# Kernel optimization log

Measured on AMD Instinct MI355X. Metric: run time of the kernel, lower is better.

## Reference

```python
import jax, jax.numpy as jnp
import numpy as np

NEG_SLOPE = 0.2  # GAT LeakyReLU slope
NEG_INF = -1e9


def setup_inputs() -> dict:
    key = jax.random.key(0)
    ks = jax.random.split(key, 5)
    B, N, D = 16, 1024, 256
    H, F = 4, 64  # heads, per-head out dim (out_dim=256)
    x = jax.random.normal(ks[0], (B, N, D), dtype=jnp.float32)
    adj = jax.random.uniform(ks[1], (B, N, N), dtype=jnp.float32)
    W = jax.random.normal(ks[2], (D, H * F), dtype=jnp.float32) * (1.0 / np.sqrt(D))
    a_src = jax.random.normal(ks[3], (H, F), dtype=jnp.float32) * (1.0 / np.sqrt(F))
    a_dst = jax.random.normal(ks[4], (H, F), dtype=jnp.float32) * (1.0 / np.sqrt(F))
    bias = jnp.zeros((H * F,), dtype=jnp.float32)
    return {"x": x, "adj": adj, "W": W, "a_src": a_src, "a_dst": a_dst, "bias": bias}


def reference(x, adj, W, a_src, a_dst, bias):
    B, N, D = x.shape
    H, F = a_src.shape
    # Linear transform per head: [B,N,H,F]
    h = jnp.einsum("bnd,dhf->bnhf", x, W.reshape(D, H, F))
    # Attention logit components: [B,N,H]
    e_src = jnp.einsum("bnhf,hf->bnh", h, a_src)
    e_dst = jnp.einsum("bnhf,hf->bnh", h, a_dst)
    # logits[b,i,j,h]: target i gathers from source j (edge = adj[b,i,j] > 0.5)
    logits = e_dst[:, :, None, :] + e_src[:, None, :, :]
    logits = jnp.where(logits >= 0, logits, NEG_SLOPE * logits)  # LeakyReLU
    mask = adj > 0.5  # [B,N,N]
    logits = jnp.where(mask[..., None], logits, NEG_INF)
    att = jax.nn.softmax(logits, axis=2)  # softmax over source neighbors j
    out = jnp.einsum("bijh,bjhf->bihf", att, h)  # aggregate
    return out.reshape(B, N, H * F) + bias  # concat heads
```

## Files before the change

### kernel.cpp

```cpp
#include <hip/hip_runtime.h>

typedef __bf16 bf16x8 __attribute__((ext_vector_type(8)));
typedef float f32x4 __attribute__((ext_vector_type(4)));

constexpr int Bsz = 16;
constexpr int Nsz = 1024;
constexpr int Dsz = 256;
constexpr int Hsz = 4;
constexpr int HFsz = 256;
constexpr int BN = Bsz * Nsz;

__device__ __forceinline__ unsigned f2bf(float f) {
    unsigned u = __float_as_uint(f);
    return (u + 0x7FFFu + ((u >> 16) & 1u)) >> 16;
}

__global__ __launch_bounds__(256) void wcvt(const float* __restrict__ Wm,
                                            unsigned short* __restrict__ WbT) {
    const int t = threadIdx.x;
    const int c = blockIdx.x * 4 + (t >> 6);
    const int d0 = (t & 63) * 4;
    const float v0 = Wm[(size_t)(d0 + 0) * HFsz + c];
    const float v1 = Wm[(size_t)(d0 + 1) * HFsz + c];
    const float v2 = Wm[(size_t)(d0 + 2) * HFsz + c];
    const float v3 = Wm[(size_t)(d0 + 3) * HFsz + c];
    uint2 pk;
    pk.x = f2bf(v0) | (f2bf(v1) << 16);
    pk.y = f2bf(v2) | (f2bf(v3) << 16);
    *(uint2*)&WbT[(size_t)c * Dsz + d0] = pk;
}

__global__ __launch_bounds__(256) void gat_h_e3(
    const float* __restrict__ x,
    const unsigned short* __restrict__ WbT,
    const float* __restrict__ a_src,
    const float* __restrict__ a_dst,
    unsigned short* __restrict__ hT,
    float* __restrict__ esrcT,
    float* __restrict__ edstT)
{
    const int n0g = blockIdx.x * 32, b = n0g >> 10, n0 = n0g & 1023;
    const int t = threadIdx.x, lane = t & 63, w = t >> 6;
    const int m = lane & 15, q = lane >> 4;

    __shared__ alignas(16) unsigned short Lds[4 * 64 * 40];

    const float4* x4 = (const float4*)(x + (size_t)n0g * Dsz);
#pragma unroll
    for (int i = 0; i < 8; ++i) {
        const int f = t + 256 * i;
        const int row = f >> 6, d4 = (f & 63) * 4;
        const float4 xv = x4[f];
        uint2 pk;
        pk.x = f2bf(xv.x) | (f2bf(xv.y) << 16);
        pk.y = f2bf(xv.z) | (f2bf(xv.w) << 16);
        *(uint2*)&Lds[row * 264 + d4] = pk;
    }
    __syncthreads();

    const unsigned short* Ab = WbT + (size_t)(w * 64 + m) * Dsz + q * 8;
    f32x4 acc[4][2];
#pragma unroll
    for (int ht = 0; ht < 4; ++ht)
#pragma unroll
        for (int nt = 0; nt < 2; ++nt) acc[ht][nt] = (f32x4){0.f, 0.f, 0.f, 0.f};

#pragma unroll
    for (int kk = 0; kk < 8; ++kk) {
        const int k0 = kk * 32;
        const bf16x8 bfr0 = *(const bf16x8*)&Lds[(0 * 16 + m) * 264 + k0 + q * 8];
        const bf16x8 bfr1 = *(const bf16x8*)&Lds[(1 * 16 + m) * 264 + k0 + q * 8];
#pragma unroll
        for (int ht = 0; ht < 4; ++ht) {
            const bf16x8 afr = *(const bf16x8*)&Ab[ht * 16 * Dsz + k0];
            acc[ht][0] = __builtin_amdgcn_mfma_f32_16x16x32_bf16(afr, bfr0, acc[ht][0], 0, 0, 0);
            acc[ht][1] = __builtin_amdgcn_mfma_f32_16x16x32_bf16(afr, bfr1, acc[ht][1], 0, 0, 0);
        }
    }

    float ps0 = 0.f, ps1 = 0.f, pd0 = 0.f, pd1 = 0.f;
#pragma unroll
    for (int ht = 0; ht < 4; ++ht)
#pragma unroll
        for (int r = 0; r < 4; ++r) {
            const float as = a_src[w * 64 + ht * 16 + q * 4 + r];
            const float ad = a_dst[w * 64 + ht * 16 + q * 4 + r];
            ps0 += acc[ht][0][r] * as;  ps1 += acc[ht][1][r] * as;
            pd0 += acc[ht][0][r] * ad;  pd1 += acc[ht][1][r] * ad;
        }
    ps0 += __shfl_xor(ps0, 16, 64); ps0 += __shfl_xor(ps0, 32, 64);
    ps1 += __shfl_xor(ps1, 16, 64); ps1 += __shfl_xor(ps1, 32, 64);
    pd0 += __shfl_xor(pd0, 16, 64); pd0 += __shfl_xor(pd0, 32, 64);
    pd1 += __shfl_xor(pd1, 16, 64); pd1 += __shfl_xor(pd1, 32, 64);
    if (q == 0) {
        const size_t eb = (size_t)(b * Hsz + w) * Nsz + n0;
        esrcT[eb + m] = ps0;  esrcT[eb + 16 + m] = ps1;
        edstT[eb + m] = pd0;  edstT[eb + 16 + m] = pd1;
    }

    __syncthreads();

#pragma unroll
    for (int ht = 0; ht < 4; ++ht)
#pragma unroll
        for (int r = 0; r < 4; ++r) {
            const int hf = ht * 16 + q * 4 + r;
            Lds[w * 2560 + hf * 40 + m]      = (unsigned short)f2bf(acc[ht][0][r]);
            Lds[w * 2560 + hf * 40 + 16 + m] = (unsigned short)f2bf(acc[ht][1][r]);
        }
#pragma unroll
    for (int s = 0; s < 4; ++s) {
        const int hf = s * 16 + (lane >> 2), ck = lane & 3;
        const bf16x8 hv = *(const bf16x8*)&Lds[w * 2560 + hf * 40 + ck * 8];
        *(bf16x8*)&hT[(size_t)(b * HFsz + w * 64 + hf) * Nsz + n0 + ck * 8] = hv;
    }
}

__global__ __launch_bounds__(64) void gat_attn3(
    const float* __restrict__ adj,
    const unsigned short* __restrict__ hT,
    const float* __restrict__ esrcT,
    const float* __restrict__ edstT,
    const float* __restrict__ bias,
    float* __restrict__ outp)
{
    const int gid = blockIdx.x;
    const int b  = gid & 15;
    const int w  = (gid >> 4) & 3;
    const int i0 = (gid >> 6) * 16;
    const int lane = threadIdx.x, m = lane & 15, q = lane >> 4;

    __shared__ alignas(16) unsigned short P_s[16][72];
    __shared__ alignas(16) float ots[16][68];

    const float* adjb = adj + (size_t)b * Nsz * Nsz + (size_t)i0 * Nsz;
    const float* esb  = esrcT + (size_t)(b * Hsz + w) * Nsz;
    const float* edb  = edstT + (size_t)(b * Hsz + w) * Nsz + i0;
    const unsigned short* hTb = hT + (size_t)(b * HFsz + w * 64 + m) * Nsz + q * 8;

    float edreg[16];
#pragma unroll
    for (int il = 0; il < 16; ++il) edreg[il] = edb[il];

    float acur[16], anxt[16];
#pragma unroll
    for (int il = 0; il < 16; ++il) acur[il] = adjb[(size_t)il * Nsz + lane];
    float escur = esb[lane], esnxt;

    float lreg[16];
#pragma unroll
    for (int il = 0; il < 16; ++il) lreg[il] = 0.f;
    f32x4 acc[4];
#pragma unroll
    for (int nt = 0; nt < 4; ++nt) acc[nt] = (f32x4){0.f, 0.f, 0.f, 0.f};

    for (int jt = 0; jt < 16; ++jt) {
        const int j0 = jt * 64;
        const int jn = (jt < 15) ? j0 + 64 : j0;
#pragma unroll
        for (int il = 0; il < 16; ++il) anxt[il] = adjb[(size_t)il * Nsz + jn + lane];
        esnxt = esb[jn + lane];

#pragma unroll
        for (int il = 0; il < 16; ++il) {
            float v = edreg[il] + escur;
            v = fmaxf(v, 0.2f * v);
            const float p = __expf(v);
            unsigned u = __float_as_uint(p);
            u = (acur[il] > 0.5f) ? u : 0u;
            P_s[il][lane] = (unsigned short)(u >> 16);
            lreg[il] += __uint_as_float(u & 0xffff0000u);
        }
        const unsigned short* hT0 = hTb + j0;
#pragma unroll
        for (int kk = 0; kk < 2; ++kk) {
            const bf16x8 afrag = *(const bf16x8*)&P_s[m][kk * 32 + q * 8];
#pragma unroll
            for (int nt = 0; nt < 4; ++nt) {
                const bf16x8 bfrag = *(const bf16x8*)&hT0[(size_t)nt * 16 * Nsz + kk * 32];
                acc[nt] = __builtin_amdgcn_mfma_f32_16x16x32_bf16(afrag, bfrag,
                                                                  acc[nt], 0, 0, 0);
            }
        }
#pragma unroll
        for (int il = 0; il < 16; ++il) acur[il] = anxt[il];
        escur = esnxt;
    }

#pragma unroll
    for (int il = 0; il < 16; ++il) {
        float l = lreg[il];
#pragma unroll
        for (int off = 32; off > 0; off >>= 1) l += __shfl_xor(l, off, 64);
        lreg[il] = l;
    }
    float linv[4];
#pragma unroll
    for (int r = 0; r < 4; ++r) {
        const float l01 = (q & 1) ? lreg[4 + r] : lreg[r];
        const float l23 = (q & 1) ? lreg[12 + r] : lreg[8 + r];
        linv[r] = 1.f / ((q & 2) ? l23 : l01);
    }

#pragma unroll
    for (int nt = 0; nt < 4; ++nt)
#pragma unroll
        for (int r = 0; r < 4; ++r)
            ots[q * 4 + r][nt * 16 + m] = acc[nt][r] * linv[r];

    const float4 bias4 = *(const float4*)&bias[w * 64 + m * 4];
#pragma unroll
    for (int s = 0; s < 4; ++s) {
        const int row = s * 4 + q;
        float4 v = *(const float4*)&ots[row][m * 4];
        v.x += bias4.x; v.y += bias4.y; v.z += bias4.z; v.w += bias4.w;
        *(float4*)&outp[(size_t)(b * Nsz + i0 + row) * HFsz + w * 64 + m * 4] = v;
    }
}

extern "C" void kernel_launch(void* const* d_in, const int* in_sizes, int n_in,
                              void* d_out, int out_size, void* d_ws, size_t ws_size,
                              hipStream_t stream) {
    const float* x     = (const float*)d_in[0];
    const float* adj   = (const float*)d_in[1];
    const float* Wm    = (const float*)d_in[2];
    const float* a_src = (const float*)d_in[3];
    const float* a_dst = (const float*)d_in[4];
    const float* bias  = (const float*)d_in[5];
    float* outp = (float*)d_out;

    unsigned short* hT  = (unsigned short*)d_ws;
    unsigned short* WbT = hT + (size_t)BN * HFsz;
    float* esrcT = (float*)(WbT + (size_t)HFsz * Dsz);
    float* edstT = esrcT + (size_t)Bsz * Hsz * Nsz;

    wcvt<<<dim3(64), dim3(256), 0, stream>>>(Wm, WbT);
    gat_h_e3<<<dim3(BN / 32), dim3(256), 0, stream>>>(x, WbT, a_src, a_dst,
                                                      hT, esrcT, edstT);
    gat_attn3<<<dim3(4096), dim3(64), 0, stream>>>(adj, hT, esrcT, edstT,
                                                   bias, outp);
}
```

Baseline: 195.2 us.

## Compute softmax row sums via MFMA with ones, prefetch hT fragments, ping-pong adj buffers

The per-row softmax denominators are now produced by an extra MFMA against a vector of bf16 ones instead of scalar accumulation and a final cross-lane shuffle reduction. The hT fragments for each tile are loaded at the top of the loop body so their latency overlaps the exp/mask work. The loop is manually unrolled by two with swapped adj register buffers, removing the register copy of the prefetched tile. This adds one MFMA per k-step and raises register pressure from holding eight fragments.

```diff
diff --git a/kernel.cpp b/kernel.cpp
--- a/kernel.cpp
+++ b/kernel.cpp
@@ -116,7 +116,7 @@
     }
 }
 
-__global__ __launch_bounds__(64) void gat_attn3(
+__global__ __launch_bounds__(64) void gat_attn4(
     const float* __restrict__ adj,
     const unsigned short* __restrict__ hT,
     const float* __restrict__ esrcT,
@@ -142,65 +142,68 @@
 #pragma unroll
     for (int il = 0; il < 16; ++il) edreg[il] = edb[il];
 
-    float acur[16], anxt[16];
-#pragma unroll
-    for (int il = 0; il < 16; ++il) acur[il] = adjb[(size_t)il * Nsz + lane];
-    float escur = esb[lane], esnxt;
-
-    float lreg[16];
-#pragma unroll
-    for (int il = 0; il < 16; ++il) lreg[il] = 0.f;
+    bf16x8 ones;
+#pragma unroll
+    for (int i = 0; i < 8; ++i)
+        ((unsigned short*)&ones)[i] = 0x3F80;
+
+    float aA[16], aB[16];
+    float esA, esB;
+#pragma unroll
+    for (int il = 0; il < 16; ++il) aA[il] = adjb[(size_t)il * Nsz + lane];
+    esA = esb[lane];
+
     f32x4 acc[4];
 #pragma unroll
     for (int nt = 0; nt < 4; ++nt) acc[nt] = (f32x4){0.f, 0.f, 0.f, 0.f};
-
-    for (int jt = 0; jt < 16; ++jt) {
+    f32x4 acc5 = (f32x4){0.f, 0.f, 0.f, 0.f};
+
+    auto body = [&](int jt, float (&ac)[16], float& esc,
+                    float (&an)[16], float& esn) {
         const int j0 = jt * 64;
+        bf16x8 bfr[8];
+#pragma unroll
+        for (int kk = 0; kk < 2; ++kk)
+#pragma unroll
+            for (int nt = 0; nt < 4; ++nt)
+                bfr[kk * 4 + nt] =
+                    *(const bf16x8*)&hTb[(size_t)nt * 16 * Nsz + j0 + kk * 32];
+
         const int jn = (jt < 15) ? j0 + 64 : j0;
 #pragma unroll
-        for (int il = 0; il < 16; ++il) anxt[il] = adjb[(size_t)il * Nsz + jn + lane];
-        esnxt = esb[jn + lane];
+        for (int il = 0; il < 16; ++il)
+            an[il] = adjb[(size_t)il * Nsz + jn + lane];
+        esn = esb[jn + lane];
 
 #pragma unroll
         for (int il = 0; il < 16; ++il) {
-            float v = edreg[il] + escur;
+            float v = edreg[il] + esc;
             v = fmaxf(v, 0.2f * v);
             const float p = __expf(v);
             unsigned u = __float_as_uint(p);
-            u = (acur[il] > 0.5f) ? u : 0u;
+            u = (ac[il] > 0.5f) ? u : 0u;
             P_s[il][lane] = (unsigned short)(u >> 16);
-            lreg[il] += __uint_as_float(u & 0xffff0000u);
-        }
-        const unsigned short* hT0 = hTb + j0;
+        }
 #pragma unroll
         for (int kk = 0; kk < 2; ++kk) {
             const bf16x8 afrag = *(const bf16x8*)&P_s[m][kk * 32 + q * 8];
 #pragma unroll
-            for (int nt = 0; nt < 4; ++nt) {
-                const bf16x8 bfrag = *(const bf16x8*)&hT0[(size_t)nt * 16 * Nsz + kk * 32];
-                acc[nt] = __builtin_amdgcn_mfma_f32_16x16x32_bf16(afrag, bfrag,
-                                                                  acc[nt], 0, 0, 0);
-            }
-        }
-#pragma unroll
-        for (int il = 0; il < 16; ++il) acur[il] = anxt[il];
-        escur = esnxt;
-    }
-
-#pragma unroll
-    for (int il = 0; il < 16; ++il) {
-        float l = lreg[il];
-#pragma unroll
-        for (int off = 32; off > 0; off >>= 1) l += __shfl_xor(l, off, 64);
-        lreg[il] = l;
-    }
+            for (int nt = 0; nt < 4; ++nt)
+                acc[nt] = __builtin_amdgcn_mfma_f32_16x16x32_bf16(
+                    afrag, bfr[kk * 4 + nt], acc[nt], 0, 0, 0);
+            acc5 = __builtin_amdgcn_mfma_f32_16x16x32_bf16(afrag, ones, acc5,
+                                                           0, 0, 0);
+        }
+    };
+
+    for (int jt = 0; jt < 16; jt += 2) {
+        body(jt, aA, esA, aB, esB);
+        body(jt + 1, aB, esB, aA, esA);
+    }
+
     float linv[4];
 #pragma unroll
-    for (int r = 0; r < 4; ++r) {
-        const float l01 = (q & 1) ? lreg[4 + r] : lreg[r];
-        const float l23 = (q & 1) ? lreg[12 + r] : lreg[8 + r];
-        linv[r] = 1.f / ((q & 2) ? l23 : l01);
-    }
+    for (int r = 0; r < 4; ++r) linv[r] = 1.f / acc5[r];
 
 #pragma unroll
     for (int nt = 0; nt < 4; ++nt)
@@ -237,6 +240,6 @@
     wcvt<<<dim3(64), dim3(256), 0, stream>>>(Wm, WbT);
     gat_h_e3<<<dim3(BN / 32), dim3(256), 0, stream>>>(x, WbT, a_src, a_dst,
                                                       hT, esrcT, edstT);
-    gat_attn3<<<dim3(4096), dim3(64), 0, stream>>>(adj, hT, esrcT, edstT,
+    gat_attn4<<<dim3(4096), dim3(64), 0, stream>>>(adj, hT, esrcT, edstT,
                                                    bias, outp);
 }
```

New measurement: 186.6 us. 1.05x faster.
